# Optimization experiments

Measured on AMD Instinct MI355X. Metric: run time of the kernel, lower is better.

The kernel has to match this reference:

```python
import jax, jax.numpy as jnp
import numpy as np

N_SRC = 50000
N_DST = 50000
IN_FEATS = 256
OUT_FEATS = 32
NUM_HEADS = 4
N_EDGES = 800000


def setup_inputs() -> dict:
    key = jax.random.key(0)
    ks = jax.random.split(key, 7)
    h_src = jax.random.normal(ks[0], (N_SRC, IN_FEATS), dtype=jnp.float32)
    h_dst = jax.random.normal(ks[1], (N_DST, IN_FEATS), dtype=jnp.float32)
    # xavier-normal-ish scaling for the shared fc weight
    W = jax.random.normal(ks[2], (IN_FEATS, NUM_HEADS * OUT_FEATS), dtype=jnp.float32) * (
        jnp.sqrt(2.0) * jnp.sqrt(2.0 / (IN_FEATS + NUM_HEADS * OUT_FEATS))
    )
    attn_l = jax.random.normal(ks[3], (NUM_HEADS, OUT_FEATS), dtype=jnp.float32) * 0.1
    attn_r = jax.random.normal(ks[4], (NUM_HEADS, OUT_FEATS), dtype=jnp.float32) * 0.1
    src_idx = jax.random.randint(ks[5], (N_EDGES,), 0, N_SRC, dtype=jnp.int32)
    dst_idx = jax.random.randint(ks[6], (N_EDGES,), 0, N_DST, dtype=jnp.int32)
    return {"h_src": h_src, "h_dst": h_dst, "W": W, "attn_l": attn_l,
            "attn_r": attn_r, "src_idx": src_idx, "dst_idx": dst_idx}


def reference(h_src, h_dst, W, attn_l, attn_r, src_idx, dst_idx):
    H, F = NUM_HEADS, OUT_FEATS
    # shared linear projection (no bias), reshape to [N, H, F]
    ft_src = (h_src @ W).reshape(-1, H, F)            # [N_src, H, F]
    ft_dst = (h_dst @ W).reshape(-1, H, F)            # [N_dst, H, F]
    # per-node attention logits, [N, H]
    el = jnp.einsum('nhf,hf->nh', ft_src, attn_l)
    er = jnp.einsum('nhf,hf->nh', ft_dst, attn_r)
    # u_add_v gather over edges, LeakyReLU(0.2) -> [E, H]
    e = jax.nn.leaky_relu(el[src_idx] + er[dst_idx], negative_slope=0.2)
    # edge softmax over incoming edges of each destination node
    smax = jax.ops.segment_max(e, dst_idx, num_segments=N_DST)   # [N_dst, H]
    e_exp = jnp.exp(e - smax[dst_idx])                           # [E, H]
    ssum = jax.ops.segment_sum(e_exp, dst_idx, num_segments=N_DST)
    a = e_exp / ssum[dst_idx]                                    # [E, H]
    # u_mul_e + scatter-sum aggregation -> [N_dst, H, F]
    msg = ft_src[src_idx] * a[:, :, None]
    rst = jax.ops.segment_sum(msg, dst_idx, num_segments=N_DST)
    return rst
```

## Files before the change

### kernel.cpp

```cpp
#include <hip/hip_runtime.h>

#define IN_FEATS 256
#define OUT_FEATS 32
#define NUM_HEADS 4
#define NHF 128

typedef __attribute__((ext_vector_type(8))) short short8;
typedef __attribute__((ext_vector_type(4))) float f32x4;

__device__ inline unsigned short f2bf(float f) {
    unsigned int u = __builtin_bit_cast(unsigned int, f);
    u = (u + 0x7fff + ((u >> 16) & 1)) >> 16;
    return (unsigned short)u;
}
__device__ inline float bfhi2f(unsigned int packed_hi) {
    return __builtin_bit_cast(float, packed_hi);
}

__global__ __launch_bounds__(256) void prep(const float* __restrict__ W,
                                            const float* __restrict__ attn_r,
                                            float* __restrict__ v,
                                            unsigned short* __restrict__ Wt) {
    if (blockIdx.x < 128) {
        int n = blockIdx.x;
        int k = threadIdx.x;
        Wt[n * 256 + k] = f2bf(W[(size_t)k * NHF + n]);
    } else {
        for (int p = threadIdx.x; p < IN_FEATS * NUM_HEADS; p += 256) {
            int k = p >> 2, h = p & 3;
            const float* wr = W + (size_t)k * NHF + h * OUT_FEATS;
            const float* ar = attn_r + h * OUT_FEATS;
            float s = 0.f;
            #pragma unroll
            for (int f = 0; f < OUT_FEATS; ++f) s += wr[f] * ar[f];
            v[p] = s;
        }
    }
}

__global__ __launch_bounds__(256) void gemm_el(const float* __restrict__ A,
                                               const unsigned short* __restrict__ Wt,
                                               const float* __restrict__ attn_l,
                                               unsigned short* __restrict__ ft16,
                                               float* __restrict__ el, int M) {
    __shared__ unsigned short WtL[128 * 256];

    const int wave = threadIdx.x >> 6;
    const int lane = threadIdx.x & 63;
    const int quad = lane >> 4;
    const int mc   = lane & 15;
    const int row_base = blockIdx.x * 64 + wave * 16;

    for (int i = threadIdx.x; i < 4096; i += 256) {
        const int n = i >> 5, c = i & 31;
        const int cs = (c + n) & 31;
        *(uint4*)(WtL + n * 256 + cs * 8) = *(const uint4*)(Wt + n * 256 + c * 8);
    }

    float al[8];
    #pragma unroll
    for (int t = 0; t < 8; ++t) al[t] = attn_l[(t >> 1) * 32 + (t & 1) * 16 + mc];

    const int rowA = min(row_base + mc, M - 1);
    const float* arow = A + (size_t)rowA * IN_FEATS;

    float4 a[8][2];
    #pragma unroll
    for (int kk = 0; kk < 8; ++kk) {
        a[kk][0] = *(const float4*)(arow + kk * 32 + quad * 8);
        a[kk][1] = *(const float4*)(arow + kk * 32 + quad * 8 + 4);
    }

    f32x4 acc[8];
    #pragma unroll
    for (int t = 0; t < 8; ++t) acc[t] = (f32x4){0.f, 0.f, 0.f, 0.f};

    __syncthreads();

    #pragma unroll
    for (int kk = 0; kk < 8; ++kk) {
        short8 af;
        af[0] = (short)f2bf(a[kk][0].x); af[1] = (short)f2bf(a[kk][0].y);
        af[2] = (short)f2bf(a[kk][0].z); af[3] = (short)f2bf(a[kk][0].w);
        af[4] = (short)f2bf(a[kk][1].x); af[5] = (short)f2bf(a[kk][1].y);
        af[6] = (short)f2bf(a[kk][1].z); af[7] = (short)f2bf(a[kk][1].w);
        #pragma unroll
        for (int t = 0; t < 8; ++t) {
            const int n = t * 16 + mc;
            const int c = ((kk << 2) + quad + n) & 31;
            const short8 bf = *(const short8*)(WtL + n * 256 + c * 8);
            acc[t] = __builtin_amdgcn_mfma_f32_16x16x32_bf16(af, bf, acc[t], 0, 0, 0);
        }
    }

    float elp[4][4];
    #pragma unroll
    for (int v = 0; v < 4; ++v)
        #pragma unroll
        for (int h = 0; h < 4; ++h) elp[v][h] = 0.f;
    #pragma unroll
    for (int v = 0; v < 4; ++v)
        #pragma unroll
        for (int t = 0; t < 8; ++t) elp[v][t >> 1] += acc[t][v] * al[t];
    #pragma unroll
    for (int v = 0; v < 4; ++v)
        #pragma unroll
        for (int h = 0; h < 4; ++h) {
            #pragma unroll
            for (int d = 1; d < 16; d <<= 1)
                elp[v][h] += __shfl_xor(elp[v][h], d, 64);
        }

    #pragma unroll
    for (int v = 0; v < 4; ++v) {
        const int rg = row_base + quad * 4 + v;
        if (rg < M) {
            unsigned short* o = ft16 + (size_t)rg * NHF;
            #pragma unroll
            for (int t = 0; t < 8; ++t) o[t * 16 + mc] = f2bf(acc[t][v]);
            if (mc < 4) {
                float ev = (mc == 0) ? elp[v][0] : (mc == 1) ? elp[v][1]
                         : (mc == 2) ? elp[v][2] : elp[v][3];
                el[(size_t)rg * 4 + mc] = ev;
            }
        }
    }
}

__global__ __launch_bounds__(256) void compute_er(const float* __restrict__ hdst,
                                                  const float* __restrict__ v,
                                                  float* __restrict__ er, int M) {
    int wid  = (blockIdx.x * blockDim.x + threadIdx.x) >> 6;
    int lane = threadIdx.x & 63;
    if (wid >= M) return;
    const float4 x = *(const float4*)(hdst + (size_t)wid * IN_FEATS + lane * 4);
    const float4* vp = (const float4*)(v + (size_t)lane * 16);
    float4 v0 = vp[0], v1 = vp[1], v2 = vp[2], v3 = vp[3];
    float a0 = x.x * v0.x + x.y * v1.x + x.z * v2.x + x.w * v3.x;
    float a1 = x.x * v0.y + x.y * v1.y + x.z * v2.y + x.w * v3.y;
    float a2 = x.x * v0.z + x.y * v1.z + x.z * v2.z + x.w * v3.z;
    float a3 = x.x * v0.w + x.y * v1.w + x.z * v2.w + x.w * v3.w;
    #pragma unroll
    for (int m = 32; m >= 1; m >>= 1) {
        a0 += __shfl_xor(a0, m, 64);
        a1 += __shfl_xor(a1, m, 64);
        a2 += __shfl_xor(a2, m, 64);
        a3 += __shfl_xor(a3, m, 64);
    }
    if (lane == 0) *(float4*)(er + (size_t)wid * 4) = make_float4(a0, a1, a2, a3);
}


__global__ __launch_bounds__(256) void bucket_hist(const int* __restrict__ dst,
                                                   int* __restrict__ bcnt, int E) {
    __shared__ int h[256];
    h[threadIdx.x] = 0;
    __syncthreads();
    for (int e = blockIdx.x * 256 + threadIdx.x; e < E; e += gridDim.x * 256)
        atomicAdd(&h[dst[e] >> 8], 1);
    __syncthreads();
    int c = h[threadIdx.x];
    if (c) atomicAdd(&bcnt[threadIdx.x], c);
}

__global__ __launch_bounds__(256) void bucket_scan(const int* __restrict__ bcnt,
                                                   int* __restrict__ bbase,
                                                   int* __restrict__ bcursor,
                                                   int* __restrict__ off, int n_dst, int E) {
    __shared__ int s[256];
    int t = threadIdx.x;
    int v = bcnt[t];
    s[t] = v;
    __syncthreads();
    #pragma unroll
    for (int d = 1; d < 256; d <<= 1) {
        int x = (t >= d) ? s[t - d] : 0;
        __syncthreads();
        s[t] += x;
        __syncthreads();
    }
    int ex = s[t] - v;
    bbase[t] = ex;
    bcursor[t] = ex;
    if (t == 255) bbase[256] = s[255];
    if (t == 0) off[n_dst] = E;
}

__global__ __launch_bounds__(256) void bin_pairs(const int* __restrict__ src,
                                                 const int* __restrict__ dst,
                                                 int* __restrict__ bcursor,
                                                 int2* __restrict__ pairs, int E) {
    __shared__ int cnt[256];
    __shared__ int basel[256];
    const int e0 = blockIdx.x * 4096;
    const int e1 = min(e0 + 4096, E);
    const int t = threadIdx.x;
    cnt[t] = 0;
    __syncthreads();
    for (int e = e0 + t; e < e1; e += 256)
        atomicAdd(&cnt[dst[e] >> 8], 1);
    __syncthreads();
    int c = cnt[t];
    basel[t] = c ? atomicAdd(&bcursor[t], c) : 0;
    __syncthreads();
    cnt[t] = 0;
    __syncthreads();
    for (int e = e0 + t; e < e1; e += 256) {
        int d = dst[e];
        int b = d >> 8;
        int o = atomicAdd(&cnt[b], 1);
        pairs[basel[b] + o] = make_int2(src[e], d);
    }
}

__global__ __launch_bounds__(256) void fine_csr(const int2* __restrict__ pairs,
                                                const int* __restrict__ bbase,
                                                int* __restrict__ off,
                                                int* __restrict__ csr_src, int n_dst) {
    __shared__ int cnt[256];
    __shared__ int cur[256];
    const int b = blockIdx.x;
    const int p0 = bbase[b], p1 = bbase[b + 1];
    const int t = threadIdx.x;
    cnt[t] = 0;
    __syncthreads();
    for (int p = p0 + t; p < p1; p += 256)
        atomicAdd(&cnt[pairs[p].y & 255], 1);
    __syncthreads();
    int v = cnt[t];
    cur[t] = v;
    __syncthreads();
    #pragma unroll
    for (int d = 1; d < 256; d <<= 1) {
        int x = (t >= d) ? cur[t - d] : 0;
        __syncthreads();
        cur[t] += x;
        __syncthreads();
    }
    int ex = cur[t] - v;
    int node = b * 256 + t;
    if (node < n_dst) off[node] = p0 + ex;
    __syncthreads();
    cur[t] = ex;
    __syncthreads();
    for (int p = p0 + t; p < p1; p += 256) {
        int2 pr = pairs[p];
        int o = atomicAdd(&cur[pr.y & 255], 1);
        csr_src[p0 + o] = pr.x;
    }
}

__global__ __launch_bounds__(256) void agg_pull(const int* __restrict__ off,
                                                const int* __restrict__ csr_src,
                                                const float* __restrict__ el,
                                                const float* __restrict__ er,
                                                const unsigned int* __restrict__ ft16p,
                                                float* __restrict__ out, int n_dst) {
    int node = (blockIdx.x * blockDim.x + threadIdx.x) >> 6;
    int lane = threadIdx.x & 63;
    if (node >= n_dst) return;
    const int h = lane >> 4;
    const float er_h = er[(size_t)node * 4 + h];
    const int start = off[node], end = off[node + 1];
    float a0 = 0.f, a1 = 0.f, sw = 0.f;
    int k = start;
    const int end4 = start + ((end - start) & ~3);
    for (; k < end4; k += 4) {
        const int s0 = csr_src[k];
        const int s1 = csr_src[k + 1];
        const int s2 = csr_src[k + 2];
        const int s3 = csr_src[k + 3];
        float x0 = el[(size_t)s0 * 4 + h];
        float x1 = el[(size_t)s1 * 4 + h];
        float x2 = el[(size_t)s2 * 4 + h];
        float x3 = el[(size_t)s3 * 4 + h];
        const unsigned int p0 = ft16p[(size_t)s0 * 64 + lane];
        const unsigned int p1 = ft16p[(size_t)s1 * 64 + lane];
        const unsigned int p2 = ft16p[(size_t)s2 * 64 + lane];
        const unsigned int p3 = ft16p[(size_t)s3 * 64 + lane];
        x0 += er_h; x0 = x0 > 0.f ? x0 : 0.2f * x0;
        x1 += er_h; x1 = x1 > 0.f ? x1 : 0.2f * x1;
        x2 += er_h; x2 = x2 > 0.f ? x2 : 0.2f * x2;
        x3 += er_h; x3 = x3 > 0.f ? x3 : 0.2f * x3;
        const float w0 = __expf(x0);
        const float w1 = __expf(x1);
        const float w2 = __expf(x2);
        const float w3 = __expf(x3);
        sw += w0 + w1 + w2 + w3;
        a0 += bfhi2f(p0 << 16) * w0 + bfhi2f(p1 << 16) * w1
            + bfhi2f(p2 << 16) * w2 + bfhi2f(p3 << 16) * w3;
        a1 += bfhi2f(p0 & 0xffff0000u) * w0 + bfhi2f(p1 & 0xffff0000u) * w1
            + bfhi2f(p2 & 0xffff0000u) * w2 + bfhi2f(p3 & 0xffff0000u) * w3;
    }
    for (; k < end; ++k) {
        const int s = csr_src[k];
        float x = el[(size_t)s * 4 + h] + er_h;
        x = x > 0.f ? x : 0.2f * x;
        const float w = __expf(x);
        const unsigned int p = ft16p[(size_t)s * 64 + lane];
        a0 += bfhi2f(p << 16) * w;
        a1 += bfhi2f(p & 0xffff0000u) * w;
        sw += w;
    }
    float2 r;
    r.x = (end > start) ? a0 / sw : 0.f;
    r.y = (end > start) ? a1 / sw : 0.f;
    *(float2*)(out + (size_t)node * NHF + 2 * lane) = r;
}

extern "C" void kernel_launch(void* const* d_in, const int* in_sizes, int n_in,
                              void* d_out, int out_size, void* d_ws, size_t ws_size,
                              hipStream_t stream) {
    const float* h_src  = (const float*)d_in[0];
    const float* h_dst  = (const float*)d_in[1];
    const float* W      = (const float*)d_in[2];
    const float* attn_l = (const float*)d_in[3];
    const float* attn_r = (const float*)d_in[4];
    const int* src_idx  = (const int*)d_in[5];
    const int* dst_idx  = (const int*)d_in[6];

    const int n_src = in_sizes[0] / IN_FEATS;
    const int n_dst = in_sizes[1] / IN_FEATS;
    const int E     = in_sizes[5];

    const int nbuck = (n_dst + 255) >> 8;

    char* ws = (char*)d_ws;
    size_t o = 0;
    float* v       = (float*)(ws + o); o += 4096;
    float* el      = (float*)(ws + o); o += (size_t)n_src * 4 * sizeof(float);
    float* er      = (float*)(ws + o); o += (size_t)n_dst * 4 * sizeof(float);
    int*   off     = (int*)(ws + o);   o += ((size_t)n_dst + 16) * sizeof(int);
    int*   bcnt    = (int*)(ws + o);   o += 256 * sizeof(int);
    int*   bbase   = (int*)(ws + o);   o += 260 * sizeof(int);
    int*   bcursor = (int*)(ws + o);   o += 256 * sizeof(int);
    unsigned short* Wt = (unsigned short*)(ws + o); o += (size_t)NHF * IN_FEATS * sizeof(unsigned short);
    int*   csr_src = (int*)(ws + o);   o += (size_t)E * sizeof(int);
    int2*  pairs   = (int2*)(ws + o);  o += (size_t)E * sizeof(int2);
    unsigned short* ft16 = (unsigned short*)(ws + o); o += (size_t)n_src * NHF * sizeof(unsigned short);

    float* out = (float*)d_out;

    (void)hipMemsetAsync(bcnt, 0, 256 * sizeof(int), stream);

    prep<<<129, 256, 0, stream>>>(W, attn_r, v, Wt);
    gemm_el<<<(n_src + 63) / 64, 256, 0, stream>>>(h_src, Wt, attn_l, ft16, el, n_src);
    compute_er<<<(n_dst + 3) / 4, 256, 0, stream>>>(h_dst, v, er, n_dst);
    bucket_hist<<<512, 256, 0, stream>>>(dst_idx, bcnt, E);
    bucket_scan<<<1, 256, 0, stream>>>(bcnt, bbase, bcursor, off, n_dst, E);
    bin_pairs<<<(E + 4095) / 4096, 256, 0, stream>>>(src_idx, dst_idx, bcursor, pairs, E);
    fine_csr<<<nbuck, 256, 0, stream>>>(pairs, bbase, off, csr_src, n_dst);
    agg_pull<<<(n_dst + 3) / 4, 256, 0, stream>>>(off, csr_src, el, er, (const unsigned int*)ft16, out, n_dst);
}
```

Before: 261.4 us.

## Process two destination nodes per wave with software-pipelined wide gathers

The aggregation kernel now maps two destination nodes to each 64-lane wave, with 32 lanes per node each loading 8 bytes (four bf16 features). Up to 32 CSR source indices are read in one coalesced load and broadcast by shuffle, and the next group of four rows is prefetched while the current one is accumulated. Edges past the first 32 fall back to a scalar loop. The aim is more bytes in flight per lane and fewer dependent index loads, paid for with masked work when the two nodes differ in degree and with higher register pressure.

```diff
diff --git a/kernel.cpp b/kernel.cpp
--- a/kernel.cpp
+++ b/kernel.cpp
@@ -254,58 +254,98 @@
                                                 const int* __restrict__ csr_src,
                                                 const float* __restrict__ el,
                                                 const float* __restrict__ er,
-                                                const unsigned int* __restrict__ ft16p,
+                                                const uint2* __restrict__ ftp,
                                                 float* __restrict__ out, int n_dst) {
-    int node = (blockIdx.x * blockDim.x + threadIdx.x) >> 6;
-    int lane = threadIdx.x & 63;
-    if (node >= n_dst) return;
-    const int h = lane >> 4;
-    const float er_h = er[(size_t)node * 4 + h];
-    const int start = off[node], end = off[node + 1];
-    float a0 = 0.f, a1 = 0.f, sw = 0.f;
-    int k = start;
-    const int end4 = start + ((end - start) & ~3);
-    for (; k < end4; k += 4) {
-        const int s0 = csr_src[k];
-        const int s1 = csr_src[k + 1];
-        const int s2 = csr_src[k + 2];
-        const int s3 = csr_src[k + 3];
-        float x0 = el[(size_t)s0 * 4 + h];
-        float x1 = el[(size_t)s1 * 4 + h];
-        float x2 = el[(size_t)s2 * 4 + h];
-        float x3 = el[(size_t)s3 * 4 + h];
-        const unsigned int p0 = ft16p[(size_t)s0 * 64 + lane];
-        const unsigned int p1 = ft16p[(size_t)s1 * 64 + lane];
-        const unsigned int p2 = ft16p[(size_t)s2 * 64 + lane];
-        const unsigned int p3 = ft16p[(size_t)s3 * 64 + lane];
-        x0 += er_h; x0 = x0 > 0.f ? x0 : 0.2f * x0;
-        x1 += er_h; x1 = x1 > 0.f ? x1 : 0.2f * x1;
-        x2 += er_h; x2 = x2 > 0.f ? x2 : 0.2f * x2;
-        x3 += er_h; x3 = x3 > 0.f ? x3 : 0.2f * x3;
-        const float w0 = __expf(x0);
-        const float w1 = __expf(x1);
-        const float w2 = __expf(x2);
-        const float w3 = __expf(x3);
-        sw += w0 + w1 + w2 + w3;
-        a0 += bfhi2f(p0 << 16) * w0 + bfhi2f(p1 << 16) * w1
-            + bfhi2f(p2 << 16) * w2 + bfhi2f(p3 << 16) * w3;
-        a1 += bfhi2f(p0 & 0xffff0000u) * w0 + bfhi2f(p1 & 0xffff0000u) * w1
-            + bfhi2f(p2 & 0xffff0000u) * w2 + bfhi2f(p3 & 0xffff0000u) * w3;
-    }
-    for (; k < end; ++k) {
+    const int wid  = (blockIdx.x * blockDim.x + threadIdx.x) >> 6;
+    const int lane = threadIdx.x & 63;
+    const int half = lane >> 5;
+    const int hl   = lane & 31;
+    const int node = wid * 2 + half;
+    const bool valid = node < n_dst;
+    const int nc = valid ? node : 0;
+    const int h  = hl >> 3;
+    const float er_h = er[nc * 4 + h];
+    const int start = off[nc];
+    const int end   = valid ? off[nc + 1] : start;
+    const int deg   = end - start;
+    const int last  = max(end - 1, 0);
+
+    const int sl = csr_src[min(start + hl, last)];
+
+    const int mdeg  = max(deg, __shfl_xor(deg, 32, 64));
+    const int iters = (min(mdeg, 32) + 3) >> 2;
+
+    float a0 = 0.f, a1 = 0.f, a2 = 0.f, a3 = 0.f, sw = 0.f;
+
+    int s0 = __shfl(sl, 0, 32), s1 = __shfl(sl, 1, 32),
+        s2 = __shfl(sl, 2, 32), s3 = __shfl(sl, 3, 32);
+    float e0 = el[s0 * 4 + h], e1 = el[s1 * 4 + h],
+          e2 = el[s2 * 4 + h], e3 = el[s3 * 4 + h];
+    uint2 q0 = ftp[s0 * 32 + hl], q1 = ftp[s1 * 32 + hl],
+          q2 = ftp[s2 * 32 + hl], q3 = ftp[s3 * 32 + hl];
+
+    for (int i = 0; i < iters; ++i) {
+        const int jn = (i + 1) << 2;
+        const int t0 = __shfl(sl, min(jn,     31), 32);
+        const int t1 = __shfl(sl, min(jn + 1, 31), 32);
+        const int t2 = __shfl(sl, min(jn + 2, 31), 32);
+        const int t3 = __shfl(sl, min(jn + 3, 31), 32);
+        const float f0 = el[t0 * 4 + h], f1 = el[t1 * 4 + h],
+                    f2 = el[t2 * 4 + h], f3 = el[t3 * 4 + h];
+        const uint2 r0 = ftp[t0 * 32 + hl], r1 = ftp[t1 * 32 + hl],
+                    r2 = ftp[t2 * 32 + hl], r3 = ftp[t3 * 32 + hl];
+
+        const int kb = start + (i << 2);
+        float x0 = e0 + er_h, x1 = e1 + er_h, x2 = e2 + er_h, x3 = e3 + er_h;
+        x0 = fmaxf(x0, 0.2f * x0);
+        x1 = fmaxf(x1, 0.2f * x1);
+        x2 = fmaxf(x2, 0.2f * x2);
+        x3 = fmaxf(x3, 0.2f * x3);
+        const float w0 = (kb     < end) ? __expf(x0) : 0.f;
+        const float w1 = (kb + 1 < end) ? __expf(x1) : 0.f;
+        const float w2 = (kb + 2 < end) ? __expf(x2) : 0.f;
+        const float w3 = (kb + 3 < end) ? __expf(x3) : 0.f;
+        sw += (w0 + w1) + (w2 + w3);
+        a0 = fmaf(bfhi2f(q0.x << 16),          w0, a0);
+        a1 = fmaf(bfhi2f(q0.x & 0xffff0000u),  w0, a1);
+        a2 = fmaf(bfhi2f(q0.y << 16),          w0, a2);
+        a3 = fmaf(bfhi2f(q0.y & 0xffff0000u),  w0, a3);
+        a0 = fmaf(bfhi2f(q1.x << 16),          w1, a0);
+        a1 = fmaf(bfhi2f(q1.x & 0xffff0000u),  w1, a1);
+        a2 = fmaf(bfhi2f(q1.y << 16),          w1, a2);
+        a3 = fmaf(bfhi2f(q1.y & 0xffff0000u),  w1, a3);
+        a0 = fmaf(bfhi2f(q2.x << 16),          w2, a0);
+        a1 = fmaf(bfhi2f(q2.x & 0xffff0000u),  w2, a1);
+        a2 = fmaf(bfhi2f(q2.y << 16),          w2, a2);
+        a3 = fmaf(bfhi2f(q2.y & 0xffff0000u),  w2, a3);
+        a0 = fmaf(bfhi2f(q3.x << 16),          w3, a0);
+        a1 = fmaf(bfhi2f(q3.x & 0xffff0000u),  w3, a1);
+        a2 = fmaf(bfhi2f(q3.y << 16),          w3, a2);
+        a3 = fmaf(bfhi2f(q3.y & 0xffff0000u),  w3, a3);
+
+        e0 = f0; e1 = f1; e2 = f2; e3 = f3;
+        q0 = r0; q1 = r1; q2 = r2; q3 = r3;
+    }
+
+    for (int k = start + 32; k < end; ++k) {
         const int s = csr_src[k];
-        float x = el[(size_t)s * 4 + h] + er_h;
-        x = x > 0.f ? x : 0.2f * x;
+        float x = el[s * 4 + h] + er_h;
+        x = fmaxf(x, 0.2f * x);
         const float w = __expf(x);
-        const unsigned int p = ft16p[(size_t)s * 64 + lane];
-        a0 += bfhi2f(p << 16) * w;
-        a1 += bfhi2f(p & 0xffff0000u) * w;
+        const uint2 q = ftp[s * 32 + hl];
         sw += w;
-    }
-    float2 r;
-    r.x = (end > start) ? a0 / sw : 0.f;
-    r.y = (end > start) ? a1 / sw : 0.f;
-    *(float2*)(out + (size_t)node * NHF + 2 * lane) = r;
+        a0 = fmaf(bfhi2f(q.x << 16),         w, a0);
+        a1 = fmaf(bfhi2f(q.x & 0xffff0000u), w, a1);
+        a2 = fmaf(bfhi2f(q.y << 16),         w, a2);
+        a3 = fmaf(bfhi2f(q.y & 0xffff0000u), w, a3);
+    }
+
+    if (valid) {
+        const float inv = (deg > 0) ? 1.f / sw : 0.f;
+        float4 r;
+        r.x = a0 * inv; r.y = a1 * inv; r.z = a2 * inv; r.w = a3 * inv;
+        *(float4*)(out + (size_t)node * NHF + hl * 4) = r;
+    }
 }
 
 extern "C" void kernel_launch(void* const* d_in, const int* in_sizes, int n_in,
@@ -350,5 +390,9 @@
     bucket_scan<<<1, 256, 0, stream>>>(bcnt, bbase, bcursor, off, n_dst, E);
     bin_pairs<<<(E + 4095) / 4096, 256, 0, stream>>>(src_idx, dst_idx, bcursor, pairs, E);
     fine_csr<<<nbuck, 256, 0, stream>>>(pairs, bbase, off, csr_src, n_dst);
-    agg_pull<<<(n_dst + 3) / 4, 256, 0, stream>>>(off, csr_src, el, er, (const unsigned int*)ft16, out, n_dst);
-}
+    {
+        const int nwave = (n_dst + 1) >> 1;
+        agg_pull<<<(nwave + 3) / 4, 256, 0, stream>>>(off, csr_src, el, er,
+                                                      (const uint2*)ft16, out, n_dst);
+    }
+}
```

Measured after the change: 258.2 us. Within noise of the previous version (-1.2%).
